# Optimization experiments

Measured on AMD Instinct MI355X. Metric: run time of the kernel, lower is better.

The kernel has to match this reference:

```python
import jax, jax.numpy as jnp
import numpy as np

B, F, N, P, G = 256, 100, 512, 512, 10  # trials, time bins, units, channels, sessions
SCALE = 1.0


def setup_inputs() -> dict:
    key = jax.random.key(0)
    k = jax.random.split(key, 6)
    x = jax.random.normal(k[0], (B, F, N), dtype=jnp.float32)
    eid = jax.random.randint(k[1], (B,), 0, G, dtype=jnp.int32)
    # Per-session stitcher Linear(N -> 2N) and projector Linear(2N -> P)
    W1 = jax.random.normal(k[2], (G, N, 2 * N), dtype=jnp.float32) / np.sqrt(N)
    b1 = jax.random.normal(k[3], (G, 2 * N), dtype=jnp.float32) * 0.01
    W2 = jax.random.normal(k[4], (G, 2 * N, P), dtype=jnp.float32) / np.sqrt(2 * N)
    b2 = jax.random.normal(k[5], (G, P), dtype=jnp.float32) * 0.01
    return {"x": x, "eid": eid, "W1": W1, "b1": b1, "W2": W2, "b2": b2}


def reference(x, eid, W1, b1, W2, b2):
    # Equivalent to the per-eid gather -> Linear -> Softsign*scale -> Linear -> scatter,
    # expressed as batched GEMMs with per-sample gathered weights (same math, vectorized).
    h = jnp.einsum('bfn,bnm->bfm', x, W1[eid]) + b1[eid][:, None, :]   # [B, F, 2N]
    h = (h / (1.0 + jnp.abs(h))) * SCALE                               # Softsign * scale
    out = jnp.einsum('bfm,bmp->bfp', h, W2[eid]) + b2[eid][:, None, :]  # [B, F, P]
    return out
```

## Files before the change

### kernel.cpp

```cpp
#include <hip/hip_runtime.h>
#include <hip/hip_bf16.h>
#include <cstdint>

typedef __attribute__((ext_vector_type(8))) short short8;
typedef __attribute__((ext_vector_type(8))) unsigned short ushort8;
typedef __attribute__((ext_vector_type(4))) float f32x4;

#define B_TRIALS 256
#define F_BINS   100
#define N_UNITS  512
#define P_CH     512
#define G_SESS   10
#define H_DIM    1024

__device__ __forceinline__ unsigned short f2bf(float f) {
  unsigned int u = __builtin_bit_cast(unsigned int, f);
  u += 0x7fffu + ((u >> 16) & 1u);
  return (unsigned short)(u >> 16);
}

__device__ __forceinline__ void gload16(const void* gsrc, void* ldst) {
  __builtin_amdgcn_global_load_lds(
      (const __attribute__((address_space(1))) unsigned int*)gsrc,
      (__attribute__((address_space(3))) unsigned int*)ldst, 16, 0, 0);
}

__global__ void cast_x(const float* __restrict__ src,
                       unsigned short* __restrict__ dst, int n8) {
  int i = blockIdx.x * blockDim.x + threadIdx.x;
  int stride = gridDim.x * blockDim.x;
  for (; i < n8; i += stride) {
    float4 v0 = ((const float4*)src)[(size_t)i * 2];
    float4 v1 = ((const float4*)src)[(size_t)i * 2 + 1];
    ushort8 w;
    w[0] = f2bf(v0.x); w[1] = f2bf(v0.y); w[2] = f2bf(v0.z); w[3] = f2bf(v0.w);
    w[4] = f2bf(v1.x); w[5] = f2bf(v1.y); w[6] = f2bf(v1.z); w[7] = f2bf(v1.w);
    ((ushort8*)dst)[i] = w;
  }
}

__global__ void cast_transpose(const float* __restrict__ src,
                               unsigned short* __restrict__ dst,
                               int K, int N) {
  __shared__ float tile[32][33];
  int g = blockIdx.z;
  int n0 = blockIdx.x * 32, k0 = blockIdx.y * 32;
  const float* s = src + (size_t)g * K * N;
  unsigned short* d = dst + (size_t)g * N * K;
  int t = threadIdx.x;
  int r = t >> 3, c = (t & 7) * 4;
  float4 v = *(const float4*)(s + (size_t)(k0 + r) * N + n0 + c);
  tile[r][c + 0] = v.x; tile[r][c + 1] = v.y;
  tile[r][c + 2] = v.z; tile[r][c + 3] = v.w;
  __syncthreads();
  ushort4 o;
  o.x = f2bf(tile[c + 0][r]);
  o.y = f2bf(tile[c + 1][r]);
  o.z = f2bf(tile[c + 2][r]);
  o.w = f2bf(tile[c + 3][r]);
  *(ushort4*)(d + (size_t)(n0 + r) * K + k0 + c) = o;
}

__global__ __launch_bounds__(256, 2) void gemm1_kernel(
    const unsigned short* __restrict__ xb, const int* __restrict__ eid,
    const unsigned short* __restrict__ W1t, const float* __restrict__ b1,
    unsigned short* __restrict__ h) {
  __shared__ __align__(16) unsigned short At[112 * 64];
  __shared__ __align__(16) unsigned short Bt[256 * 64];
  int b = blockIdx.y;
  int ncol0 = blockIdx.x * 256;
  int g = eid[b];
  int tid = threadIdx.x;
  int wv = tid >> 6, lane = tid & 63;
  int lr = lane & 15, lg = lane >> 4;
  int wcol0 = wv * 64;

  const unsigned short* Wg = W1t + (size_t)g * H_DIM * N_UNITS + (size_t)ncol0 * N_UNITS;
  const unsigned short* xg = xb + (size_t)b * F_BINS * N_UNITS;

  f32x4 zero = {0.f, 0.f, 0.f, 0.f};
  f32x4 acc[7][4];
#pragma unroll
  for (int i = 0; i < 7; i++)
#pragma unroll
    for (int j = 0; j < 4; j++) acc[i][j] = zero;

  for (int k0 = 0; k0 < N_UNITS; k0 += 64) {
    __syncthreads();
#pragma unroll
    for (int r8 = 0; r8 < 8; r8++) {
      int idx = r8 * 256 + tid;
      int col = idx >> 3, s = idx & 7;
      int ks = s ^ (col & 7);
      gload16(Wg + (size_t)col * N_UNITS + k0 + ks * 8,
              &Bt[(r8 * 256 + (tid & 192)) * 8]);
    }
#pragma unroll
    for (int r4 = 0; r4 < 4; r4++) {
      int idx = r4 * 256 + tid;
      if (idx < 896) {
        int row = idx >> 3, s = idx & 7;
        int ks = s ^ (row & 7);
        int srow = row < F_BINS ? row : F_BINS - 1;
        gload16(xg + (size_t)srow * N_UNITS + k0 + ks * 8,
                &At[(r4 * 256 + (tid & 192)) * 8]);
      }
    }
    asm volatile("s_waitcnt vmcnt(0) lgkmcnt(0)" ::: "memory");
    __syncthreads();
#pragma unroll
    for (int kk = 0; kk < 2; kk++) {
      int kslot = kk * 4 + lg;
      short8 af[7];
#pragma unroll
      for (int mf = 0; mf < 7; mf++) {
        int row = mf * 16 + lr;
        af[mf] = *(const short8*)&At[row * 64 + ((kslot ^ (row & 7)) * 8)];
      }
#pragma unroll
      for (int nf = 0; nf < 4; nf++) {
        int col = wcol0 + nf * 16 + lr;
        short8 bv = *(const short8*)&Bt[col * 64 + ((kslot ^ (col & 7)) * 8)];
#pragma unroll
        for (int mf = 0; mf < 7; mf++)
          acc[mf][nf] = __builtin_amdgcn_mfma_f32_16x16x32_bf16(af[mf], bv, acc[mf][nf], 0, 0, 0);
      }
    }
  }
  float b1v[4];
#pragma unroll
  for (int nf = 0; nf < 4; nf++)
    b1v[nf] = b1[(size_t)g * H_DIM + ncol0 + wcol0 + nf * 16 + lr];
#pragma unroll
  for (int mf = 0; mf < 7; mf++) {
#pragma unroll
    for (int r = 0; r < 4; r++) {
      int row = mf * 16 + lg * 4 + r;
      if (row < F_BINS) {
        size_t ho = ((size_t)b * F_BINS + row) * H_DIM + ncol0 + wcol0 + lr;
#pragma unroll
        for (int nf = 0; nf < 4; nf++) {
          float v = acc[mf][nf][r] + b1v[nf];
          v = v / (1.0f + fabsf(v));
          h[ho + nf * 16] = f2bf(v);
        }
      }
    }
  }
}

__global__ __launch_bounds__(256, 2) void gemm2_kernel(
    const unsigned short* __restrict__ h, const int* __restrict__ eid,
    const unsigned short* __restrict__ W2t, const float* __restrict__ b2,
    float* __restrict__ out) {
  __shared__ __align__(16) unsigned short At[112 * 64];
  __shared__ __align__(16) unsigned short Bt[256 * 64];
  int b = blockIdx.y;
  int pcol0 = blockIdx.x * 256;
  int g = eid[b];
  int tid = threadIdx.x;
  int wv = tid >> 6, lane = tid & 63;
  int lr = lane & 15, lg = lane >> 4;
  int wcol0 = wv * 64;

  const unsigned short* Wg = W2t + (size_t)g * P_CH * H_DIM + (size_t)pcol0 * H_DIM;
  const unsigned short* hg = h + (size_t)b * F_BINS * H_DIM;

  f32x4 zero = {0.f, 0.f, 0.f, 0.f};
  f32x4 acc[7][4];
#pragma unroll
  for (int i = 0; i < 7; i++)
#pragma unroll
    for (int j = 0; j < 4; j++) acc[i][j] = zero;

  for (int k0 = 0; k0 < H_DIM; k0 += 64) {
    __syncthreads();
#pragma unroll
    for (int r8 = 0; r8 < 8; r8++) {
      int idx = r8 * 256 + tid;
      int col = idx >> 3, s = idx & 7;
      int ks = s ^ (col & 7);
      gload16(Wg + (size_t)col * H_DIM + k0 + ks * 8,
              &Bt[(r8 * 256 + (tid & 192)) * 8]);
    }
#pragma unroll
    for (int r4 = 0; r4 < 4; r4++) {
      int idx = r4 * 256 + tid;
      if (idx < 896) {
        int row = idx >> 3, s = idx & 7;
        int ks = s ^ (row & 7);
        int srow = row < F_BINS ? row : F_BINS - 1;
        gload16(hg + (size_t)srow * H_DIM + k0 + ks * 8,
                &At[(r4 * 256 + (tid & 192)) * 8]);
      }
    }
    asm volatile("s_waitcnt vmcnt(0) lgkmcnt(0)" ::: "memory");
    __syncthreads();
#pragma unroll
    for (int kk = 0; kk < 2; kk++) {
      int kslot = kk * 4 + lg;
      short8 af[7];
#pragma unroll
      for (int mf = 0; mf < 7; mf++) {
        int row = mf * 16 + lr;
        af[mf] = *(const short8*)&At[row * 64 + ((kslot ^ (row & 7)) * 8)];
      }
#pragma unroll
      for (int nf = 0; nf < 4; nf++) {
        int col = wcol0 + nf * 16 + lr;
        short8 bv = *(const short8*)&Bt[col * 64 + ((kslot ^ (col & 7)) * 8)];
#pragma unroll
        for (int mf = 0; mf < 7; mf++)
          acc[mf][nf] = __builtin_amdgcn_mfma_f32_16x16x32_bf16(af[mf], bv, acc[mf][nf], 0, 0, 0);
      }
    }
  }
  float b2v[4];
#pragma unroll
  for (int nf = 0; nf < 4; nf++)
    b2v[nf] = b2[(size_t)g * P_CH + pcol0 + wcol0 + nf * 16 + lr];
#pragma unroll
  for (int mf = 0; mf < 7; mf++) {
#pragma unroll
    for (int r = 0; r < 4; r++) {
      int row = mf * 16 + lg * 4 + r;
      if (row < F_BINS) {
        size_t oo = ((size_t)b * F_BINS + row) * P_CH + pcol0 + wcol0 + lr;
#pragma unroll
        for (int nf = 0; nf < 4; nf++)
          out[oo + nf * 16] = acc[mf][nf][r] + b2v[nf];
      }
    }
  }
}

extern "C" void kernel_launch(void* const* d_in, const int* in_sizes, int n_in,
                              void* d_out, int out_size, void* d_ws, size_t ws_size,
                              hipStream_t stream) {
  const float* x  = (const float*)d_in[0];
  const int* eid  = (const int*)d_in[1];
  const float* W1 = (const float*)d_in[2];
  const float* b1 = (const float*)d_in[3];
  const float* W2 = (const float*)d_in[4];
  const float* b2 = (const float*)d_in[5];
  float* out = (float*)d_out;

  unsigned short* W1t = (unsigned short*)d_ws;
  unsigned short* W2t = W1t + (size_t)G_SESS * H_DIM * N_UNITS;
  unsigned short* h   = W2t + (size_t)G_SESS * P_CH * H_DIM;
  unsigned short* xb  = (unsigned short*)d_out;

  cast_x<<<2048, 256, 0, stream>>>(x, xb, B_TRIALS * F_BINS * N_UNITS / 8);
  cast_transpose<<<dim3(H_DIM / 32, N_UNITS / 32, G_SESS), 256, 0, stream>>>(W1, W1t, N_UNITS, H_DIM);
  cast_transpose<<<dim3(P_CH / 32, H_DIM / 32, G_SESS), 256, 0, stream>>>(W2, W2t, H_DIM, P_CH);
  gemm1_kernel<<<dim3(4, B_TRIALS), 256, 0, stream>>>(xb, eid, W1t, b1, h);
  gemm2_kernel<<<dim3(2, B_TRIALS), 256, 0, stream>>>(h, eid, W2t, b2, out);
}
```

Baseline: 107.7 us.

## Group rows by session into 256-row tiles with a 4-stage pipelined grouped GEMM

Adds a planner kernel that sorts trials by session and builds a row map and tile metadata, so each GEMM block handles 256 rows that share one weight matrix instead of one 100-row trial padded to 112. Both GEMMs become a single templated grouped kernel with 512 threads, a 4-deep LDS ring of global_load_lds stages, and set-priority around the MFMA blocks. The intent is to raise weight reuse, cut padding waste, and overlap loads with compute. The cost is an extra single-block planner launch, indirect row gathers, scattered output writes, and a fixed grid of 110 tiles in which some blocks exit early.

```diff
diff --git a/kernel.cpp b/kernel.cpp
--- a/kernel.cpp
+++ b/kernel.cpp
@@ -12,6 +12,8 @@
 #define P_CH     512
 #define G_SESS   10
 #define H_DIM    1024
+#define TOT_ROWS (B_TRIALS * F_BINS)
+#define NT_MAX   110
 
 __device__ __forceinline__ unsigned short f2bf(float f) {
   unsigned int u = __builtin_bit_cast(unsigned int, f);
@@ -23,6 +25,52 @@
   __builtin_amdgcn_global_load_lds(
       (const __attribute__((address_space(1))) unsigned int*)gsrc,
       (__attribute__((address_space(3))) unsigned int*)ldst, 16, 0, 0);
+}
+
+__global__ void planner(const int* __restrict__ eid, int* __restrict__ rowmap,
+                        int* __restrict__ tile_meta) {
+  __shared__ int e[B_TRIALS], cnt[G_SESS], off[G_SESS], groff[G_SESS + 1], perm[B_TRIALS];
+  int t = threadIdx.x;
+  e[t] = eid[t];
+  if (t < G_SESS) cnt[t] = 0;
+  __syncthreads();
+  atomicAdd(&cnt[e[t]], 1);
+  __syncthreads();
+  if (t == 0) {
+    int s = 0, r = 0;
+    for (int g = 0; g < G_SESS; g++) {
+      off[g] = s; s += cnt[g];
+      groff[g] = r; r += cnt[g] * F_BINS;
+    }
+    groff[G_SESS] = r;
+  }
+  __syncthreads();
+  int g = e[t], rank = 0;
+  for (int j = 0; j < t; j++) rank += (e[j] == g);
+  perm[off[g] + rank] = t;
+  __syncthreads();
+  for (int i = t; i < TOT_ROWS; i += 256) {
+    int gg = 0;
+    while (gg + 1 < G_SESS && i >= groff[gg + 1]) gg++;
+    int loc = i - groff[gg];
+    rowmap[i] = perm[off[gg] + loc / F_BINS] * F_BINS + loc % F_BINS;
+  }
+  if (t == 0) {
+    int ti = 0;
+    for (int g2 = 0; g2 < G_SESS; g2++) {
+      int rows = cnt[g2] * F_BINS;
+      int base = groff[g2];
+      for (int r0 = 0; r0 < rows; r0 += 256) {
+        tile_meta[ti * 3 + 0] = g2;
+        tile_meta[ti * 3 + 1] = base + r0;
+        tile_meta[ti * 3 + 2] = (rows - r0 < 256) ? (rows - r0) : 256;
+        ti++;
+      }
+    }
+    for (; ti < NT_MAX; ti++) {
+      tile_meta[ti * 3 + 0] = -1; tile_meta[ti * 3 + 1] = 0; tile_meta[ti * 3 + 2] = 0;
+    }
+  }
 }
 
 __global__ void cast_x(const float* __restrict__ src,
@@ -61,176 +109,137 @@
   *(ushort4*)(d + (size_t)(n0 + r) * K + k0 + c) = o;
 }
 
-__global__ __launch_bounds__(256, 2) void gemm1_kernel(
-    const unsigned short* __restrict__ xb, const int* __restrict__ eid,
-    const unsigned short* __restrict__ W1t, const float* __restrict__ b1,
-    unsigned short* __restrict__ h) {
-  __shared__ __align__(16) unsigned short At[112 * 64];
-  __shared__ __align__(16) unsigned short Bt[256 * 64];
-  int b = blockIdx.y;
-  int ncol0 = blockIdx.x * 256;
-  int g = eid[b];
-  int tid = threadIdx.x;
-  int wv = tid >> 6, lane = tid & 63;
-  int lr = lane & 15, lg = lane >> 4;
-  int wcol0 = wv * 64;
-
-  const unsigned short* Wg = W1t + (size_t)g * H_DIM * N_UNITS + (size_t)ncol0 * N_UNITS;
-  const unsigned short* xg = xb + (size_t)b * F_BINS * N_UNITS;
-
-  f32x4 zero = {0.f, 0.f, 0.f, 0.f};
-  f32x4 acc[7][4];
-#pragma unroll
-  for (int i = 0; i < 7; i++)
-#pragma unroll
-    for (int j = 0; j < 4; j++) acc[i][j] = zero;
-
-  for (int k0 = 0; k0 < N_UNITS; k0 += 64) {
-    __syncthreads();
-#pragma unroll
-    for (int r8 = 0; r8 < 8; r8++) {
-      int idx = r8 * 256 + tid;
-      int col = idx >> 3, s = idx & 7;
-      int ks = s ^ (col & 7);
-      gload16(Wg + (size_t)col * N_UNITS + k0 + ks * 8,
-              &Bt[(r8 * 256 + (tid & 192)) * 8]);
-    }
-#pragma unroll
-    for (int r4 = 0; r4 < 4; r4++) {
-      int idx = r4 * 256 + tid;
-      if (idx < 896) {
-        int row = idx >> 3, s = idx & 7;
-        int ks = s ^ (row & 7);
-        int srow = row < F_BINS ? row : F_BINS - 1;
-        gload16(xg + (size_t)srow * N_UNITS + k0 + ks * 8,
-                &At[(r4 * 256 + (tid & 192)) * 8]);
-      }
-    }
-    asm volatile("s_waitcnt vmcnt(0) lgkmcnt(0)" ::: "memory");
-    __syncthreads();
-#pragma unroll
-    for (int kk = 0; kk < 2; kk++) {
-      int kslot = kk * 4 + lg;
-      short8 af[7];
-#pragma unroll
-      for (int mf = 0; mf < 7; mf++) {
-        int row = mf * 16 + lr;
-        af[mf] = *(const short8*)&At[row * 64 + ((kslot ^ (row & 7)) * 8)];
-      }
-#pragma unroll
-      for (int nf = 0; nf < 4; nf++) {
-        int col = wcol0 + nf * 16 + lr;
-        short8 bv = *(const short8*)&Bt[col * 64 + ((kslot ^ (col & 7)) * 8)];
-#pragma unroll
-        for (int mf = 0; mf < 7; mf++)
-          acc[mf][nf] = __builtin_amdgcn_mfma_f32_16x16x32_bf16(af[mf], bv, acc[mf][nf], 0, 0, 0);
-      }
-    }
-  }
-  float b1v[4];
-#pragma unroll
-  for (int nf = 0; nf < 4; nf++)
-    b1v[nf] = b1[(size_t)g * H_DIM + ncol0 + wcol0 + nf * 16 + lr];
-#pragma unroll
-  for (int mf = 0; mf < 7; mf++) {
-#pragma unroll
-    for (int r = 0; r < 4; r++) {
-      int row = mf * 16 + lg * 4 + r;
-      if (row < F_BINS) {
-        size_t ho = ((size_t)b * F_BINS + row) * H_DIM + ncol0 + wcol0 + lr;
-#pragma unroll
-        for (int nf = 0; nf < 4; nf++) {
-          float v = acc[mf][nf][r] + b1v[nf];
-          v = v / (1.0f + fabsf(v));
-          h[ho + nf * 16] = f2bf(v);
+
+#define STAGE(kt) do {                                                      \
+    int _b = (kt) & 3; int _k0 = (kt) * 32;                                 \
+    gload16(b0p + _k0, &Bb[_b][(size_t)(tid & 448) * 8]);                   \
+    gload16(b1p + _k0, &Bb[_b][(size_t)(512 + (tid & 448)) * 8]);           \
+    gload16(a0p + _k0, &Ab[_b][(size_t)(tid & 448) * 8]);                   \
+    gload16(a1p + _k0, &Ab[_b][(size_t)(512 + (tid & 448)) * 8]);           \
+  } while (0)
+
+#define KSTEP(kt, VM) do {                                                  \
+    asm volatile("s_waitcnt vmcnt(" #VM ")" ::: "memory");                  \
+    __builtin_amdgcn_s_barrier();                                           \
+    asm volatile("" ::: "memory");                                          \
+    const unsigned short* Ap = &Ab[(kt) & 3][0];                            \
+    const unsigned short* Bp = &Bb[(kt) & 3][0];                            \
+    short8 av[8], bv[4];                                                    \
+    _Pragma("unroll")                                                       \
+    for (int m = 0; m < 8; m++) {                                           \
+      int rw = wm * 128 + m * 16 + lr;                                      \
+      av[m] = *(const short8*)&Ap[rw * 32 + sl8];                           \
+    }                                                                       \
+    _Pragma("unroll")                                                       \
+    for (int n = 0; n < 4; n++) {                                           \
+      int cl = wn * 64 + n * 16 + lr;                                       \
+      bv[n] = *(const short8*)&Bp[cl * 32 + sl8];                           \
+    }                                                                       \
+    __builtin_amdgcn_s_setprio(1);                                          \
+    _Pragma("unroll")                                                       \
+    for (int n = 0; n < 4; n++)                                             \
+      _Pragma("unroll")                                                     \
+      for (int m = 0; m < 8; m++)                                           \
+        acc[m][n] = __builtin_amdgcn_mfma_f32_16x16x32_bf16(av[m], bv[n], acc[m][n], 0, 0, 0); \
+    __builtin_amdgcn_s_setprio(0);                                          \
+    asm volatile("" ::: "memory");                                          \
+    __builtin_amdgcn_s_barrier();                                           \
+  } while (0)
+
+template<int KTOT, int NOUT, bool IS2>
+__global__ __launch_bounds__(512, 2) void gemm_grouped(
+    const unsigned short* __restrict__ Asrc,
+    const unsigned short* __restrict__ Wt,
+    const float* __restrict__ bias,
+    const int* __restrict__ rowmap,
+    const int* __restrict__ tile_meta,
+    unsigned short* __restrict__ hout,
+    float* __restrict__ out) {
+  __shared__ __align__(16) unsigned short Ab[4][256 * 32];
+  __shared__ __align__(16) unsigned short Bb[4][256 * 32];
+
+  const int mt = blockIdx.x;
+  const int g = tile_meta[mt * 3 + 0];
+  if (g < 0) return;
+  const int row0 = tile_meta[mt * 3 + 1];
+  const int valid = tile_meta[mt * 3 + 2];
+  const int ncol0 = blockIdx.y * 256;
+
+  const int tid = threadIdx.x;
+  const int lane = tid & 63;
+  const int w = tid >> 6;
+  const int wm = w >> 2, wn = w & 3;
+  const int lr = lane & 15, lq = lane >> 4;
+  const int sl8 = ((lq ^ ((lr >> 1) & 3)) * 8);
+
+  const unsigned short* Wg = Wt + (size_t)g * NOUT * KTOT + (size_t)ncol0 * KTOT;
+  const unsigned short *b0p, *b1p, *a0p, *a1p;
+  {
+    int idx0 = tid, idx1 = 512 + tid;
+    int c0 = idx0 >> 2, q0 = idx0 & 3, ks0 = q0 ^ ((c0 >> 1) & 3);
+    int c1 = idx1 >> 2, q1 = idx1 & 3, ks1 = q1 ^ ((c1 >> 1) & 3);
+    b0p = Wg + (size_t)c0 * KTOT + ks0 * 8;
+    b1p = Wg + (size_t)c1 * KTOT + ks1 * 8;
+    int rr0 = row0 + c0; if (rr0 > TOT_ROWS - 1) rr0 = TOT_ROWS - 1;
+    int rr1 = row0 + c1; if (rr1 > TOT_ROWS - 1) rr1 = TOT_ROWS - 1;
+    int sr0 = IS2 ? rr0 : rowmap[rr0];
+    int sr1 = IS2 ? rr1 : rowmap[rr1];
+    a0p = Asrc + (size_t)sr0 * KTOT + ks0 * 8;
+    a1p = Asrc + (size_t)sr1 * KTOT + ks1 * 8;
+  }
+
+  f32x4 acc[8][4];
+#pragma unroll
+  for (int m = 0; m < 8; m++)
+#pragma unroll
+    for (int n = 0; n < 4; n++) acc[m][n] = (f32x4){0.f, 0.f, 0.f, 0.f};
+
+  constexpr int NK = KTOT / 32;
+  STAGE(0); STAGE(1); STAGE(2);
+#pragma unroll 4
+  for (int kt = 0; kt < NK - 3; kt++) {
+    STAGE(kt + 3);
+    KSTEP(kt, 12);
+  }
+  KSTEP(NK - 3, 8);
+  KSTEP(NK - 2, 4);
+  KSTEP(NK - 1, 0);
+
+  float bv4[4];
+#pragma unroll
+  for (int n = 0; n < 4; n++)
+    bv4[n] = bias[(size_t)g * NOUT + ncol0 + wn * 64 + n * 16 + lr];
+
+  if (!IS2) {
+#pragma unroll
+    for (int m = 0; m < 8; m++)
+#pragma unroll
+      for (int r4 = 0; r4 < 4; r4++) {
+        int lrow = wm * 128 + m * 16 + lq * 4 + r4;
+        if (lrow < valid) {
+          size_t base = (size_t)(row0 + lrow) * H_DIM + ncol0 + wn * 64 + lr;
+#pragma unroll
+          for (int n = 0; n < 4; n++) {
+            float v = acc[m][n][r4] + bv4[n];
+            v = v / (1.0f + fabsf(v));
+            hout[base + n * 16] = f2bf(v);
+          }
         }
       }
-    }
-  }
-}
-
-__global__ __launch_bounds__(256, 2) void gemm2_kernel(
-    const unsigned short* __restrict__ h, const int* __restrict__ eid,
-    const unsigned short* __restrict__ W2t, const float* __restrict__ b2,
-    float* __restrict__ out) {
-  __shared__ __align__(16) unsigned short At[112 * 64];
-  __shared__ __align__(16) unsigned short Bt[256 * 64];
-  int b = blockIdx.y;
-  int pcol0 = blockIdx.x * 256;
-  int g = eid[b];
-  int tid = threadIdx.x;
-  int wv = tid >> 6, lane = tid & 63;
-  int lr = lane & 15, lg = lane >> 4;
-  int wcol0 = wv * 64;
-
-  const unsigned short* Wg = W2t + (size_t)g * P_CH * H_DIM + (size_t)pcol0 * H_DIM;
-  const unsigned short* hg = h + (size_t)b * F_BINS * H_DIM;
-
-  f32x4 zero = {0.f, 0.f, 0.f, 0.f};
-  f32x4 acc[7][4];
-#pragma unroll
-  for (int i = 0; i < 7; i++)
-#pragma unroll
-    for (int j = 0; j < 4; j++) acc[i][j] = zero;
-
-  for (int k0 = 0; k0 < H_DIM; k0 += 64) {
-    __syncthreads();
-#pragma unroll
-    for (int r8 = 0; r8 < 8; r8++) {
-      int idx = r8 * 256 + tid;
-      int col = idx >> 3, s = idx & 7;
-      int ks = s ^ (col & 7);
-      gload16(Wg + (size_t)col * H_DIM + k0 + ks * 8,
-              &Bt[(r8 * 256 + (tid & 192)) * 8]);
-    }
-#pragma unroll
-    for (int r4 = 0; r4 < 4; r4++) {
-      int idx = r4 * 256 + tid;
-      if (idx < 896) {
-        int row = idx >> 3, s = idx & 7;
-        int ks = s ^ (row & 7);
-        int srow = row < F_BINS ? row : F_BINS - 1;
-        gload16(hg + (size_t)srow * H_DIM + k0 + ks * 8,
-                &At[(r4 * 256 + (tid & 192)) * 8]);
+  } else {
+#pragma unroll
+    for (int m = 0; m < 8; m++)
+#pragma unroll
+      for (int r4 = 0; r4 < 4; r4++) {
+        int lrow = wm * 128 + m * 16 + lq * 4 + r4;
+        if (lrow < valid) {
+          int orow = rowmap[row0 + lrow];
+          size_t base = (size_t)orow * P_CH + ncol0 + wn * 64 + lr;
+#pragma unroll
+          for (int n = 0; n < 4; n++)
+            out[base + n * 16] = acc[m][n][r4] + bv4[n];
+        }
       }
-    }
-    asm volatile("s_waitcnt vmcnt(0) lgkmcnt(0)" ::: "memory");
-    __syncthreads();
-#pragma unroll
-    for (int kk = 0; kk < 2; kk++) {
-      int kslot = kk * 4 + lg;
-      short8 af[7];
-#pragma unroll
-      for (int mf = 0; mf < 7; mf++) {
-        int row = mf * 16 + lr;
-        af[mf] = *(const short8*)&At[row * 64 + ((kslot ^ (row & 7)) * 8)];
-      }
-#pragma unroll
-      for (int nf = 0; nf < 4; nf++) {
-        int col = wcol0 + nf * 16 + lr;
-        short8 bv = *(const short8*)&Bt[col * 64 + ((kslot ^ (col & 7)) * 8)];
-#pragma unroll
-        for (int mf = 0; mf < 7; mf++)
-          acc[mf][nf] = __builtin_amdgcn_mfma_f32_16x16x32_bf16(af[mf], bv, acc[mf][nf], 0, 0, 0);
-      }
-    }
-  }
-  float b2v[4];
-#pragma unroll
-  for (int nf = 0; nf < 4; nf++)
-    b2v[nf] = b2[(size_t)g * P_CH + pcol0 + wcol0 + nf * 16 + lr];
-#pragma unroll
-  for (int mf = 0; mf < 7; mf++) {
-#pragma unroll
-    for (int r = 0; r < 4; r++) {
-      int row = mf * 16 + lg * 4 + r;
-      if (row < F_BINS) {
-        size_t oo = ((size_t)b * F_BINS + row) * P_CH + pcol0 + wcol0 + lr;
-#pragma unroll
-        for (int nf = 0; nf < 4; nf++)
-          out[oo + nf * 16] = acc[mf][nf][r] + b2v[nf];
-      }
-    }
   }
 }
 
@@ -248,11 +257,16 @@
   unsigned short* W1t = (unsigned short*)d_ws;
   unsigned short* W2t = W1t + (size_t)G_SESS * H_DIM * N_UNITS;
   unsigned short* h   = W2t + (size_t)G_SESS * P_CH * H_DIM;
-  unsigned short* xb  = (unsigned short*)d_out;
-
+  int* rowmap    = (int*)(h + (size_t)TOT_ROWS * H_DIM);
+  int* tile_meta = rowmap + TOT_ROWS;
+  unsigned short* xb = (unsigned short*)d_out;
+
+  planner<<<1, 256, 0, stream>>>(eid, rowmap, tile_meta);
   cast_x<<<2048, 256, 0, stream>>>(x, xb, B_TRIALS * F_BINS * N_UNITS / 8);
   cast_transpose<<<dim3(H_DIM / 32, N_UNITS / 32, G_SESS), 256, 0, stream>>>(W1, W1t, N_UNITS, H_DIM);
   cast_transpose<<<dim3(P_CH / 32, H_DIM / 32, G_SESS), 256, 0, stream>>>(W2, W2t, H_DIM, P_CH);
-  gemm1_kernel<<<dim3(4, B_TRIALS), 256, 0, stream>>>(xb, eid, W1t, b1, h);
-  gemm2_kernel<<<dim3(2, B_TRIALS), 256, 0, stream>>>(h, eid, W2t, b2, out);
-}
+  gemm_grouped<N_UNITS, H_DIM, false><<<dim3(NT_MAX, 4), 512, 0, stream>>>(
+      xb, W1t, b1, rowmap, tile_meta, h, out);
+  gemm_grouped<H_DIM, P_CH, true><<<dim3(NT_MAX, 2), 512, 0, stream>>>(
+      h, W2t, b2, rowmap, tile_meta, h, out);
+}
```

New measurement: 150.0 us. 1.39x slower.
